# Kernel tuning notes

Hardware: AMD Instinct MI355X
Metric: run time of the kernel (lower is better)

Reference implementation:

```python
import jax, jax.numpy as jnp
import numpy as np

N, LQ, C, M, L, P = 8, 2048, 256, 8, 4, 4
DH = C // M  # 32
LENS = (2048, 1024, 512, 256)


def setup_inputs() -> dict:
    key = jax.random.key(0)
    ks = jax.random.split(key, 8)
    s = 1.0 / np.sqrt(C)
    return {
        "query": jax.random.normal(ks[0], (N, LQ, C), jnp.float32),
        "reference_points": jax.random.uniform(ks[1], (N, LQ, L, 1), jnp.float32),
        "input_flatten": jax.random.normal(ks[2], (N, sum(LENS), C), jnp.float32),
        "temporal_lens": np.array(LENS, np.int64),
        "level_start_index": np.array([0, 2048, 3072, 3584], np.int64),
        "W_off": jax.random.normal(ks[3], (C, M * L * P), jnp.float32) * 0.01,
        "b_off": jax.random.normal(ks[4], (M * L * P,), jnp.float32),
        "W_attn": jax.random.normal(ks[5], (C, M * L * P), jnp.float32) * 0.01,
        "b_attn": jnp.zeros((M * L * P,), jnp.float32),
        "W_val": jax.random.normal(ks[6], (C, C), jnp.float32) * s,
        "b_val": jnp.zeros((C,), jnp.float32),
        "W_out": jax.random.normal(ks[7], (C, C), jnp.float32) * s,
        "b_out": jnp.zeros((C,), jnp.float32),
    }


def _deform_core(value, lens, loc, attn):
    # value: (N, S, M, DH); loc, attn: (N, LQ, M, L, P); loc in normalized [0,1] coords.
    # Equivalent to per-level F.grid_sample (bilinear, zeros padding, align_corners=False)
    # on a 1xT image: pixel position = loc*T - 0.5; the y-coord 0.5 lands exactly on row 0.
    outs = []
    start = 0
    for l, T in enumerate(lens):
        v = value[:, start:start + T].transpose(0, 2, 1, 3)  # (N, M, T, DH)
        start += T
        pos = loc[..., l, :] * T - 0.5                       # (N, LQ, M, P)
        x0f = jnp.floor(pos)
        frac = pos - x0f
        x0 = x0f.astype(jnp.int32)

        def gather(idx):
            i = jnp.clip(idx, 0, T - 1).transpose(0, 2, 1, 3).reshape(N, M, LQ * P, 1)
            return jnp.take_along_axis(v, i, axis=2).reshape(N, M, LQ, P, DH)

        in0 = ((x0 >= 0) & (x0 < T)).astype(value.dtype)
        in1 = ((x0 + 1 >= 0) & (x0 + 1 < T)).astype(value.dtype)
        w0 = ((1.0 - frac) * in0).transpose(0, 2, 1, 3)[..., None]  # (N, M, LQ, P, 1)
        w1 = (frac * in1).transpose(0, 2, 1, 3)[..., None]
        outs.append(gather(x0) * w0 + gather(x0 + 1) * w1)          # (N, M, LQ, P, DH)
    sampled = jnp.stack(outs, axis=3)          # (N, M, LQ, L, P, DH)
    aw = attn.transpose(0, 2, 1, 3, 4)         # (N, M, LQ, L, P)
    return jnp.einsum('nmqlpd,nmqlp->nqmd', sampled, aw).reshape(N, LQ, C)


def reference(query, reference_points, input_flatten, temporal_lens, level_start_index,
              W_off, b_off, W_attn, b_attn, W_val, b_val, W_out, b_out):
    lens = [int(t) for t in np.asarray(temporal_lens)[:L]]  # static per-level lengths
    value = (input_flatten @ W_val + b_val).reshape(N, -1, M, DH)
    off = (query @ W_off + b_off).reshape(N, LQ, M, L, P)
    attn = jax.nn.softmax((query @ W_attn + b_attn).reshape(N, LQ, M, L * P), axis=-1)
    attn = attn.reshape(N, LQ, M, L, P)
    norm = jnp.asarray(lens, query.dtype)                    # offset_normalizer (L,)
    loc = reference_points[:, :, None, :, None, 0] + off / norm[None, None, None, :, None]
    out = _deform_core(value, lens, loc, attn)
    out = out @ W_out + b_out
    return out, loc, attn
```

## Files before the change

kernel.cpp:

```cpp
#include <hip/hip_runtime.h>
#include <hip/hip_bf16.h>
#include <math.h>

#define NB 8
#define LQ 2048
#define SSUM 3840

typedef unsigned short ushort_t;
typedef unsigned int uint_t;
typedef __attribute__((ext_vector_type(8))) short bf16x8;
typedef __attribute__((ext_vector_type(4))) float f32x4;

__device__ __forceinline__ ushort_t f2bf(float f) {
  __hip_bfloat16 h = __float2bfloat16(f);
  return *reinterpret_cast<ushort_t*>(&h);
}
__device__ __forceinline__ uint_t pk2bf(float lo, float hi) {
  float2 t; t.x = lo; t.y = hi;
  __hip_bfloat162 h = __float22bfloat162_rn(t);
  return *reinterpret_cast<uint_t*>(&h);
}
__device__ __forceinline__ float bf2f_lo(uint_t u) {
  union { uint_t u32; float f; } x;
  x.u32 = u << 16;
  return x.f;
}
__device__ __forceinline__ float bf2f_hi(uint_t u) {
  union { uint_t u32; float f; } x;
  x.u32 = u & 0xffff0000u;
  return x.f;
}
__device__ __forceinline__ void ld_lds16(const void* g, void* l) {
  __builtin_amdgcn_global_load_lds(
      (const __attribute__((address_space(1))) void*)g,
      (__attribute__((address_space(3))) void*)l, 16, 0, 0);
}

__global__ __launch_bounds__(256) void prep_conv(
    const float* __restrict__ W_val, const float* __restrict__ W_off,
    const float* __restrict__ W_attn, const float* __restrict__ W_out,
    const float* __restrict__ in_flat, const float* __restrict__ query,
    ushort_t* __restrict__ BtVal, ushort_t* __restrict__ BtOA,
    ushort_t* __restrict__ BtOut,
    ushort_t* in_bf, ushort_t* q_bf) {
  const int b = blockIdx.x, t = threadIdx.x;
  if (b < 768) {
    if (b < 256) { BtVal[b * 256 + t] = f2bf(W_val[(size_t)t * 256 + b]); return; }
    if (b < 512) { int n = b - 256; BtOut[n * 256 + t] = f2bf(W_out[(size_t)t * 256 + n]); return; }
    if (b < 640) { int n = b - 512; BtOA[n * 256 + t] = f2bf(W_off[(size_t)t * 128 + n]); return; }
    int n = b - 640; BtOA[(128 + n) * 256 + t] = f2bf(W_attn[(size_t)t * 128 + n]);
    return;
  }
  size_t gid = (size_t)(b - 768) * 256 + t;
  const float* src; ushort_t* dst; size_t e;
  if (gid < 983040u) { src = in_flat; dst = in_bf; e = gid * 8; }
  else               { src = query;   dst = q_bf;  e = (gid - 983040u) * 8; }
  float4 f0 = *(const float4*)(src + e);
  float4 f1 = *(const float4*)(src + e + 4);
  uint4 c;
  c.x = pk2bf(f0.x, f0.y);
  c.y = pk2bf(f0.z, f0.w);
  c.z = pk2bf(f1.x, f1.y);
  c.w = pk2bf(f1.z, f1.w);
  *(uint4*)(dst + e) = c;
}

__global__ __launch_bounds__(256) void gemm_fused(
    int job_base,
    const ushort_t* in_bf,
    const ushort_t* qcore,
    const ushort_t* __restrict__ BtVal, const ushort_t* __restrict__ BtOA,
    const ushort_t* __restrict__ BtOut,
    const float* __restrict__ b_val, const float* __restrict__ b_off,
    const float* __restrict__ b_attn, const float* __restrict__ b_out,
    ushort_t* value, float* __restrict__ loc,
    float* __restrict__ attn, float* __restrict__ out) {
  __shared__ ushort_t Ab[3][64][32];
  __shared__ ushort_t Bb[3][256][32];

  const int job = job_base + blockIdx.x;

  const ushort_t* Asrc;
  const ushort_t* Bt;
  const float* bias_lo; const float* bias_hi;
  int bm, cstride;
  ushort_t* Cb = nullptr;
  float* Cf_lo = nullptr; float* Cf_hi = nullptr;

  if (job < 480) {
    bm = job * 64; Asrc = in_bf; Bt = BtVal;
    bias_lo = b_val; bias_hi = b_val + 128; Cb = value; cstride = 256;
  } else if (job < 736) {
    bm = (job - 480) * 64; Asrc = qcore; Bt = BtOA;
    bias_lo = b_off; bias_hi = b_attn; Cf_lo = loc; Cf_hi = attn; cstride = 128;
  } else {
    bm = (job - 736) * 64; Asrc = qcore; Bt = BtOut;
    bias_lo = b_out; bias_hi = b_out + 128; Cf_lo = out; Cf_hi = out + 128;
    cstride = 256;
  }

  const int tid = threadIdx.x;
  const int lane = tid & 63;
  const int wv = tid >> 6;
  const int quad = lane >> 4;
  const int l16 = lane & 15;
  const int wm = (wv >> 1) * 32;
  const int wn = (wv & 1) * 128;
  const int drow = lane >> 2;
  const int dk = (lane & 3) * 8;

  f32x4 acc[2][8];
#pragma unroll
  for (int i = 0; i < 2; ++i)
#pragma unroll
    for (int j = 0; j < 8; ++j) acc[i][j] = (f32x4)(0.f);

  auto stage = [&](int sb, int k0) {
    ld_lds16(Asrc + (size_t)(bm + wv * 16 + drow) * 256 + k0 + dk,
             &Ab[sb][wv * 16 + drow][dk]);
#pragma unroll
    for (int c = 0; c < 4; ++c)
      ld_lds16(Bt + (size_t)(wv * 64 + c * 16 + drow) * 256 + k0 + dk,
               &Bb[sb][wv * 64 + c * 16 + drow][dk]);
  };

  stage(0, 0);
  stage(1, 32);

#pragma unroll
  for (int it = 0; it < 8; ++it) {
    if (it < 7) asm volatile("s_waitcnt vmcnt(5)" ::: "memory");
    else        asm volatile("s_waitcnt vmcnt(0)" ::: "memory");
    __builtin_amdgcn_s_barrier();
    __builtin_amdgcn_sched_barrier(0);
    if (it < 6) stage((it + 2) % 3, (it + 2) * 32);

    const int sb = it % 3;
    bf16x8 af[2], bfr[8];
#pragma unroll
    for (int mi = 0; mi < 2; ++mi)
      af[mi] = *(const bf16x8*)&Ab[sb][wm + mi * 16 + l16][quad * 8];
#pragma unroll
    for (int ni = 0; ni < 8; ++ni)
      bfr[ni] = *(const bf16x8*)&Bb[sb][wn + ni * 16 + l16][quad * 8];
#pragma unroll
    for (int mi = 0; mi < 2; ++mi)
#pragma unroll
      for (int ni = 0; ni < 8; ++ni)
        acc[mi][ni] = __builtin_amdgcn_mfma_f32_16x16x32_bf16(af[mi], bfr[ni], acc[mi][ni], 0, 0, 0);
  }

  const int hi = wv & 1;
  const float* bias = hi ? bias_hi : bias_lo;
  ushort_t* Cbw = Cb ? (Cb + (hi ? 128 : 0)) : nullptr;
  float* Cfw = hi ? Cf_hi : Cf_lo;

#pragma unroll
  for (int ni = 0; ni < 8; ++ni) {
    int cc = ni * 16 + l16;
    float bv = bias[cc];
#pragma unroll
    for (int mi = 0; mi < 2; ++mi) {
      f32x4 v = acc[mi][ni];
      int rbase = bm + wm + mi * 16 + quad * 4;
#pragma unroll
      for (int r = 0; r < 4; ++r) {
        float o = v[r] + bv;
        size_t idx = (size_t)(rbase + r) * cstride + cc;
        if (Cbw) Cbw[idx] = f2bf(o);
        else     Cfw[idx] = o;
      }
    }
  }
}

__global__ __launch_bounds__(256) void deform_fused(
    const ushort_t* __restrict__ value,
    float* __restrict__ locbuf,
    float* __restrict__ attnbuf,
    const float* __restrict__ refp,
    ushort_t* __restrict__ core) {
  const int tid = threadIdx.x;
  const int nq0 = blockIdx.x * 4;
  const int n = nq0 >> 11;

  __shared__ float4 sp[512];

#pragma unroll
  for (int j = 0; j < 2; ++j) {
    int s = tid + j * 256;
    int q = s >> 7;
    int r = s & 127;
    int m = r >> 4;
    int lp = r & 15;
    int l = lp >> 2;
    int T = 2048 >> l;
    int start = 4096 - (4096 >> l);
    float rn = (float)(1 << l) * (1.0f / 2048.0f);

    float lraw = locbuf[(size_t)nq0 * 128 + s];
    float logit = attnbuf[(size_t)nq0 * 128 + s];
    float lv = refp[(size_t)(nq0 + q) * 4 + l] + lraw * rn;
    locbuf[(size_t)nq0 * 128 + s] = lv;

    float mx = logit;
    mx = fmaxf(mx, __shfl_xor(mx, 1, 64));
    mx = fmaxf(mx, __shfl_xor(mx, 2, 64));
    mx = fmaxf(mx, __shfl_xor(mx, 4, 64));
    mx = fmaxf(mx, __shfl_xor(mx, 8, 64));
    float e = __expf(logit - mx);
    float sm = e;
    sm += __shfl_xor(sm, 1, 64);
    sm += __shfl_xor(sm, 2, 64);
    sm += __shfl_xor(sm, 4, 64);
    sm += __shfl_xor(sm, 8, 64);
    float aw = e / sm;
    attnbuf[(size_t)nq0 * 128 + s] = aw;

    float pos = lv * (float)T - 0.5f;
    float x0f = floorf(pos);
    float fr = pos - x0f;
    int x0 = (int)x0f;
    float w0 = ((unsigned)x0 < (unsigned)T) ? (1.f - fr) * aw : 0.f;
    float w1 = ((unsigned)(x0 + 1) < (unsigned)T) ? fr * aw : 0.f;
    int i0 = min(max(x0, 0), T - 1);
    int i1 = min(max(x0 + 1, 0), T - 1);
    float4 pr;
    pr.x = w0;
    pr.y = w1;
    pr.z = __int_as_float((start + i0) * 256);
    pr.w = __int_as_float((start + i1) * 256);
    sp[q * 128 + lp * 8 + m] = pr;
  }
  __syncthreads();

  const int q = tid >> 6;
  const int t64 = tid & 63;
  const int m = t64 >> 3;
  const int g = t64 & 7;
  const ushort_t* vbase = value + (size_t)n * (SSUM * 256) + m * 32 + g * 4;

  float a0 = 0.f, a1 = 0.f, a2 = 0.f, a3 = 0.f;
#pragma unroll
  for (int lp = 0; lp < 16; ++lp) {
    float4 pr = sp[q * 128 + lp * 8 + m];
    int o0 = __float_as_int(pr.z);
    int o1 = __float_as_int(pr.w);
    uint2 u0 = *(const uint2*)(vbase + o0);
    uint2 u1 = *(const uint2*)(vbase + o1);
    a0 += pr.x * bf2f_lo(u0.x) + pr.y * bf2f_lo(u1.x);
    a1 += pr.x * bf2f_hi(u0.x) + pr.y * bf2f_hi(u1.x);
    a2 += pr.x * bf2f_lo(u0.y) + pr.y * bf2f_lo(u1.y);
    a3 += pr.x * bf2f_hi(u0.y) + pr.y * bf2f_hi(u1.y);
  }
  uint2 outp;
  outp.x = (uint_t)f2bf(a0) | ((uint_t)f2bf(a1) << 16);
  outp.y = (uint_t)f2bf(a2) | ((uint_t)f2bf(a3) << 16);
  *(uint2*)&core[(size_t)(nq0 + q) * 256 + m * 32 + g * 4] = outp;
}

extern "C" void kernel_launch(void* const* d_in, const int* in_sizes, int n_in,
                              void* d_out, int out_size, void* d_ws, size_t ws_size,
                              hipStream_t stream) {
  const float* query    = (const float*)d_in[0];
  const float* refpts   = (const float*)d_in[1];
  const float* in_flat  = (const float*)d_in[2];
  const float* W_off  = (const float*)d_in[5];
  const float* b_off  = (const float*)d_in[6];
  const float* W_attn = (const float*)d_in[7];
  const float* b_attn = (const float*)d_in[8];
  const float* W_val  = (const float*)d_in[9];
  const float* b_val  = (const float*)d_in[10];
  const float* W_out  = (const float*)d_in[11];
  const float* b_out  = (const float*)d_in[12];

  float* out  = (float*)d_out;
  float* loc  = out + (size_t)NB * LQ * 256;
  float* attn = loc + (size_t)NB * LQ * 128;

  ushort_t* value = (ushort_t*)d_ws;
  ushort_t* core  = value + (size_t)NB * SSUM * 256;
  ushort_t* BtVal = core + (size_t)NB * LQ * 256;
  ushort_t* BtOA  = BtVal + 65536;
  ushort_t* BtOut = BtOA + 65536;

  const int Mq = NB * LQ;

  prep_conv<<<768 + 5888, 256, 0, stream>>>(
      W_val, W_off, W_attn, W_out, in_flat, query,
      BtVal, BtOA, BtOut, value, core);

  gemm_fused<<<736, 256, 0, stream>>>(
      0, value, core, BtVal, BtOA, BtOut,
      b_val, b_off, b_attn, b_out, value, loc, attn, out);

  deform_fused<<<Mq / 4, 256, 0, stream>>>(value, loc, attn, refpts, core);

  gemm_fused<<<256, 256, 0, stream>>>(
      736, value, core, BtVal, BtOA, BtOut,
      b_val, b_off, b_attn, b_out, value, loc, attn, out);
}
```

Baseline: 168.5 us.

## Fuse fp32-to-bf16 input conversion into GEMM A-tile loading and swizzle deform blocks

The separate pass that converted input_flatten and query to bf16 is removed. The first GEMM now reads fp32 A tiles straight into registers, converts them and writes them into LDS inside a register-staged pipeline, while B still goes through direct-to-LDS loads. This drops a full global write and re-read of the converted activations, at the cost of register staging and an extra lgkmcnt wait each iteration. The deform kernel also remaps block indices so that consecutive blocks are spread across batches, which may change cache locality.

```diff
diff --git a/kernel.cpp b/kernel.cpp
--- a/kernel.cpp
+++ b/kernel.cpp
@@ -36,39 +36,23 @@
       (__attribute__((address_space(3))) void*)l, 16, 0, 0);
 }
 
-__global__ __launch_bounds__(256) void prep_conv(
+__global__ __launch_bounds__(256) void prep(
     const float* __restrict__ W_val, const float* __restrict__ W_off,
     const float* __restrict__ W_attn, const float* __restrict__ W_out,
-    const float* __restrict__ in_flat, const float* __restrict__ query,
     ushort_t* __restrict__ BtVal, ushort_t* __restrict__ BtOA,
-    ushort_t* __restrict__ BtOut,
-    ushort_t* in_bf, ushort_t* q_bf) {
+    ushort_t* __restrict__ BtOut) {
   const int b = blockIdx.x, t = threadIdx.x;
-  if (b < 768) {
-    if (b < 256) { BtVal[b * 256 + t] = f2bf(W_val[(size_t)t * 256 + b]); return; }
-    if (b < 512) { int n = b - 256; BtOut[n * 256 + t] = f2bf(W_out[(size_t)t * 256 + n]); return; }
-    if (b < 640) { int n = b - 512; BtOA[n * 256 + t] = f2bf(W_off[(size_t)t * 128 + n]); return; }
-    int n = b - 640; BtOA[(128 + n) * 256 + t] = f2bf(W_attn[(size_t)t * 128 + n]);
-    return;
-  }
-  size_t gid = (size_t)(b - 768) * 256 + t;
-  const float* src; ushort_t* dst; size_t e;
-  if (gid < 983040u) { src = in_flat; dst = in_bf; e = gid * 8; }
-  else               { src = query;   dst = q_bf;  e = (gid - 983040u) * 8; }
-  float4 f0 = *(const float4*)(src + e);
-  float4 f1 = *(const float4*)(src + e + 4);
-  uint4 c;
-  c.x = pk2bf(f0.x, f0.y);
-  c.y = pk2bf(f0.z, f0.w);
-  c.z = pk2bf(f1.x, f1.y);
-  c.w = pk2bf(f1.z, f1.w);
-  *(uint4*)(dst + e) = c;
-}
-
+  if (b < 256) { BtVal[b * 256 + t] = f2bf(W_val[(size_t)t * 256 + b]); return; }
+  if (b < 512) { int n = b - 256; BtOut[n * 256 + t] = f2bf(W_out[(size_t)t * 256 + n]); return; }
+  if (b < 640) { int n = b - 512; BtOA[n * 256 + t] = f2bf(W_off[(size_t)t * 128 + n]); return; }
+  int n = b - 640; BtOA[(128 + n) * 256 + t] = f2bf(W_attn[(size_t)t * 128 + n]);
+}
+
+template <bool AF32>
 __global__ __launch_bounds__(256) void gemm_fused(
     int job_base,
-    const ushort_t* in_bf,
-    const ushort_t* qcore,
+    const float* __restrict__ in_flat, const float* __restrict__ query,
+    const ushort_t* core,
     const ushort_t* __restrict__ BtVal, const ushort_t* __restrict__ BtOA,
     const ushort_t* __restrict__ BtOut,
     const float* __restrict__ b_val, const float* __restrict__ b_off,
@@ -80,7 +64,8 @@
 
   const int job = job_base + blockIdx.x;
 
-  const ushort_t* Asrc;
+  const float* Afp = nullptr;
+  const ushort_t* Abf = nullptr;
   const ushort_t* Bt;
   const float* bias_lo; const float* bias_hi;
   int bm, cstride;
@@ -88,13 +73,13 @@
   float* Cf_lo = nullptr; float* Cf_hi = nullptr;
 
   if (job < 480) {
-    bm = job * 64; Asrc = in_bf; Bt = BtVal;
+    bm = job * 64; Afp = in_flat; Bt = BtVal;
     bias_lo = b_val; bias_hi = b_val + 128; Cb = value; cstride = 256;
   } else if (job < 736) {
-    bm = (job - 480) * 64; Asrc = qcore; Bt = BtOA;
+    bm = (job - 480) * 64; Afp = query; Bt = BtOA;
     bias_lo = b_off; bias_hi = b_attn; Cf_lo = loc; Cf_hi = attn; cstride = 128;
   } else {
-    bm = (job - 736) * 64; Asrc = qcore; Bt = BtOut;
+    bm = (job - 736) * 64; Abf = core; Bt = BtOut;
     bias_lo = b_out; bias_hi = b_out + 128; Cf_lo = out; Cf_hi = out + 128;
     cstride = 256;
   }
@@ -115,25 +100,59 @@
 #pragma unroll
     for (int j = 0; j < 8; ++j) acc[i][j] = (f32x4)(0.f);
 
-  auto stage = [&](int sb, int k0) {
-    ld_lds16(Asrc + (size_t)(bm + wv * 16 + drow) * 256 + k0 + dk,
-             &Ab[sb][wv * 16 + drow][dk]);
+  auto stageB = [&](int sb, int k0) {
 #pragma unroll
     for (int c = 0; c < 4; ++c)
       ld_lds16(Bt + (size_t)(wv * 64 + c * 16 + drow) * 256 + k0 + dk,
                &Bb[sb][wv * 64 + c * 16 + drow][dk]);
   };
-
-  stage(0, 0);
-  stage(1, 32);
+  auto stageA_dma = [&](int sb, int k0) {
+    ld_lds16(Abf + (size_t)(bm + wv * 16 + drow) * 256 + k0 + dk,
+             &Ab[sb][wv * 16 + drow][dk]);
+  };
+  float4 ra[2][2];
+  auto issueA = [&](int ph, int k0) {
+    const float* gp = Afp + (size_t)(bm + wv * 16 + drow) * 256 + k0 + dk;
+    ra[ph][0] = *(const float4*)gp;
+    ra[ph][1] = *(const float4*)(gp + 4);
+  };
+  auto writeA = [&](int ph, int sb) {
+    uint4 c;
+    c.x = pk2bf(ra[ph][0].x, ra[ph][0].y);
+    c.y = pk2bf(ra[ph][0].z, ra[ph][0].w);
+    c.z = pk2bf(ra[ph][1].x, ra[ph][1].y);
+    c.w = pk2bf(ra[ph][1].z, ra[ph][1].w);
+    *(uint4*)&Ab[sb][wv * 16 + drow][dk] = c;
+  };
+
+  if (AF32) {
+    issueA(0, 0);   stageB(0, 0);
+    issueA(1, 32);  stageB(1, 32);
+    writeA(0, 0);
+  } else {
+    stageA_dma(0, 0);  stageB(0, 0);
+    stageA_dma(1, 32); stageB(1, 32);
+  }
 
 #pragma unroll
   for (int it = 0; it < 8; ++it) {
-    if (it < 7) asm volatile("s_waitcnt vmcnt(5)" ::: "memory");
-    else        asm volatile("s_waitcnt vmcnt(0)" ::: "memory");
+    if (it < 7) {
+      if (AF32) asm volatile("s_waitcnt vmcnt(4)" ::: "memory");
+      else      asm volatile("s_waitcnt vmcnt(5)" ::: "memory");
+    } else {
+      asm volatile("s_waitcnt vmcnt(0)" ::: "memory");
+    }
+    asm volatile("s_waitcnt lgkmcnt(0)" ::: "memory");
     __builtin_amdgcn_s_barrier();
     __builtin_amdgcn_sched_barrier(0);
-    if (it < 6) stage((it + 2) % 3, (it + 2) * 32);
+
+    if (it < 6) {
+      if (AF32) issueA(it & 1, (it + 2) * 32);
+      else      stageA_dma((it + 2) % 3, (it + 2) * 32);
+      stageB((it + 2) % 3, (it + 2) * 32);
+    }
+    if (AF32 && it < 7)
+      writeA((it ^ 1) & 1, (it + 1) % 3);
 
     const int sb = it % 3;
     bf16x8 af[2], bfr[8];
@@ -181,7 +200,9 @@
     const float* __restrict__ refp,
     ushort_t* __restrict__ core) {
   const int tid = threadIdx.x;
-  const int nq0 = blockIdx.x * 4;
+  const int bid = blockIdx.x;
+  const int swz = (bid & 7) * 512 + (bid >> 3);
+  const int nq0 = swz * 4;
   const int n = nq0 >> 11;
 
   __shared__ float4 sp[512];
@@ -286,17 +307,15 @@
 
   const int Mq = NB * LQ;
 
-  prep_conv<<<768 + 5888, 256, 0, stream>>>(
-      W_val, W_off, W_attn, W_out, in_flat, query,
-      BtVal, BtOA, BtOut, value, core);
-
-  gemm_fused<<<736, 256, 0, stream>>>(
-      0, value, core, BtVal, BtOA, BtOut,
+  prep<<<768, 256, 0, stream>>>(W_val, W_off, W_attn, W_out, BtVal, BtOA, BtOut);
+
+  gemm_fused<true><<<736, 256, 0, stream>>>(
+      0, in_flat, query, core, BtVal, BtOA, BtOut,
       b_val, b_off, b_attn, b_out, value, loc, attn, out);
 
   deform_fused<<<Mq / 4, 256, 0, stream>>>(value, loc, attn, refpts, core);
 
-  gemm_fused<<<256, 256, 0, stream>>>(
-      736, value, core, BtVal, BtOA, BtOut,
+  gemm_fused<false><<<256, 256, 0, stream>>>(
+      736, in_flat, query, core, BtVal, BtOA, BtOut,
       b_val, b_off, b_attn, b_out, value, loc, attn, out);
 }
```

After: 167.4 us. About the same (-0.7%).
